# Kernel optimization log

Hardware: AMD Instinct MI355X
Metric: run time of the kernel (lower is better)

## Reference

```python
import jax, jax.numpy as jnp
import numpy as np

D_MODEL = 1024
NUM_HEADS = 16
DEPTH = D_MODEL // NUM_HEADS
B, S = 2, 2048


def setup_inputs() -> dict:
    key = jax.random.key(0)
    ks = jax.random.split(key, 12)
    std = 1.0 / np.sqrt(D_MODEL)
    inp = {
        "q": jax.random.normal(ks[0], (B, S, D_MODEL), dtype=jnp.float32),
        "k": jax.random.normal(ks[1], (B, S, D_MODEL), dtype=jnp.float32),
        "v": jax.random.normal(ks[2], (B, S, D_MODEL), dtype=jnp.float32),
        "mask": jax.random.randint(ks[3], (B, 1, 1, S), 0, 2, dtype=jnp.int32),
        "wq": jax.random.normal(ks[4], (D_MODEL, D_MODEL), dtype=jnp.float32) * std,
        "bq": jnp.zeros((D_MODEL,), dtype=jnp.float32),
        "wk": jax.random.normal(ks[5], (D_MODEL, D_MODEL), dtype=jnp.float32) * std,
        "bk": jnp.zeros((D_MODEL,), dtype=jnp.float32),
        "wv": jax.random.normal(ks[6], (D_MODEL, D_MODEL), dtype=jnp.float32) * std,
        "bv": jnp.zeros((D_MODEL,), dtype=jnp.float32),
        "wo": jax.random.normal(ks[7], (D_MODEL, D_MODEL), dtype=jnp.float32) * std,
        "bo": jnp.zeros((D_MODEL,), dtype=jnp.float32),
    }
    return inp


def _split_heads(x):
    # (B, S, D) -> (B, H, S, depth)
    b, s, _ = x.shape
    return x.reshape(b, s, NUM_HEADS, DEPTH).transpose(0, 2, 1, 3)


def reference(q, k, v, mask, wq, bq, wk, bk, wv, bv, wo, bo):
    qh = _split_heads(q @ wq + bq)   # (B,H,S,depth)
    kh = _split_heads(k @ wk + bk)
    vh = _split_heads(v @ wv + bv)
    scale = 1.0 / jnp.sqrt(jnp.float32(DEPTH))
    logits = jnp.einsum("bhqd,bhkd->bhqk", qh, kh) * scale  # (B,H,Sq,Sk)
    logits = logits + mask.astype(logits.dtype) * -1e9
    attn = jax.nn.softmax(logits, axis=-1)
    out = jnp.einsum("bhqk,bhkd->bhqd", attn, vh)  # (B,H,Sq,depth)
    out = out.transpose(0, 2, 1, 3).reshape(q.shape[0], -1, D_MODEL)
    return out @ wo + bo
```

## Files before the change

kernel.cpp:

```cpp
#include <hip/hip_runtime.h>
#include <hip/hip_bf16.h>
#include <stdint.h>


typedef __bf16 bf16;
typedef __bf16 bf16x8 __attribute__((ext_vector_type(8)));
typedef __bf16 bf16x4 __attribute__((ext_vector_type(4)));
typedef float  f32x4  __attribute__((ext_vector_type(4)));

#define D_MODEL 1024
#define S_LEN   2048
#define NH      16
#define DEPTH   64

#define LOG2E   1.4426950408889634f
#define QSCALE  (0.125f * LOG2E)
#define SMAX    20.0f
#define MPEN    (-30000.0f)

__device__ __forceinline__ void gload_lds16(const void* g, void* l) {
  __builtin_amdgcn_global_load_lds(
      (__attribute__((address_space(1))) void*)g,
      (__attribute__((address_space(3))) void*)l,
      16, 0, 0);
}

__global__ void probe_dtype(const uint32_t* __restrict__ qw, int* __restrict__ flag)
{
  const int t = threadIdx.x;
  int c = 0;
  for (int i = 0; i < 4; ++i) {
    uint32_t w = qw[t * 4 + i];
    uint32_t e = (w >> 7) & 0xFF;
    c += (e >= 90 && e <= 150) ? 1 : 0;
  }
  for (int s = 1; s < 64; s <<= 1) c += __shfl_xor(c, s);
  if (t == 0) *flag = (c > 160) ? 1 : 0;
}

__global__ __launch_bounds__(256) void prep_qkv(
    const void* __restrict__ q, const void* __restrict__ k,
    const void* __restrict__ v,
    bf16* __restrict__ qb, bf16* __restrict__ kb, bf16* __restrict__ vb,
    const int* __restrict__ flagp)
{
  if (*flagp) return;
  const void* src; bf16* dst;
  switch (blockIdx.z) {
    case 0:  src = q; dst = qb; break;
    case 1:  src = k; dst = kb; break;
    default: src = v; dst = vb; break;
  }
  const size_t idx = ((size_t)blockIdx.x * 256 + threadIdx.x) * 8;
  const float* s = (const float*)src + idx;
  f32x4 a = *(const f32x4*)(s);
  f32x4 b = *(const f32x4*)(s + 4);
  bf16x8 o;
  for (int i = 0; i < 4; ++i) { o[i] = (bf16)a[i]; o[4 + i] = (bf16)b[i]; }
  *(bf16x8*)(dst + idx) = o;
}

__global__ __launch_bounds__(256) void prep_w(
    const void* __restrict__ w0, const void* __restrict__ w1,
    const void* __restrict__ w2, const void* __restrict__ w3,
    bf16* __restrict__ t0, bf16* __restrict__ t1,
    bf16* __restrict__ t2, bf16* __restrict__ t3,
    const int* __restrict__ flagp)
{
  const int flag = *flagp;
  const void* W; bf16* T;
  switch (blockIdx.z) {
    case 0:  W = w0; T = t0; break;
    case 1:  W = w1; T = t1; break;
    case 2:  W = w2; T = t2; break;
    default: W = w3; T = t3; break;
  }
  const float sc = (blockIdx.z == 0) ? QSCALE : 1.0f;
  __shared__ float tile[32][33];
  const int tx = threadIdx.x;
  const int x0 = blockIdx.x * 32;
  const int y0 = blockIdx.y * 32;
  for (int i = threadIdx.y; i < 32; i += 8) {
    const size_t gi = (size_t)(y0 + i) * D_MODEL + x0 + tx;
    tile[i][tx] = flag ? (float)((const bf16*)W)[gi] : ((const float*)W)[gi];
  }
  __syncthreads();
  for (int i = threadIdx.y; i < 32; i += 8)
    T[(size_t)(x0 + i) * D_MODEL + y0 + tx] = (bf16)(tile[tx][i] * sc);
}

__global__ __launch_bounds__(256) void prep_bias(
    const void* __restrict__ b0, const void* __restrict__ b1,
    const void* __restrict__ b2, const void* __restrict__ b3,
    bf16* __restrict__ o0, bf16* __restrict__ o1,
    bf16* __restrict__ o2, bf16* __restrict__ o3,
    const int* __restrict__ flagp)
{
  const int flag = *flagp;
  const void* B; bf16* O;
  switch (blockIdx.x) {
    case 0:  B = b0; O = o0; break;
    case 1:  B = b1; O = o1; break;
    case 2:  B = b2; O = o2; break;
    default: B = b3; O = o3; break;
  }
  const float sc = (blockIdx.x == 0) ? QSCALE : 1.0f;
  for (int j = 0; j < 4; ++j) {
    const int i = threadIdx.x + j * 256;
    const float v = flag ? (float)((const bf16*)B)[i] : ((const float*)B)[i];
    O[i] = (bf16)(v * sc);
  }
}

struct GArgs {
  const bf16* A;
  const void* Araw;
  const bf16* BT;
  const bf16* bias;
  void* out;
  int mode;
};

__global__ __launch_bounds__(256) void gemm_bt(GArgs g0, GArgs g1, GArgs g2,
                                               const int* __restrict__ flagp)
{
  GArgs g = (blockIdx.z == 0) ? g0 : ((blockIdx.z == 1) ? g1 : g2);
  const int flag = *flagp;
  const bf16* A = flag ? (const bf16*)g.Araw : g.A;

  __shared__ __align__(16) bf16 As[128 * 32];
  __shared__ __align__(16) bf16 Bs[128 * 32];
  const int tid  = threadIdx.x;
  const int wave = tid >> 6, lane = tid & 63;
  const int quad = lane >> 4, l16 = lane & 15;
  const int m0 = blockIdx.y * 128, n0 = blockIdx.x * 128;
  const int wm = (wave >> 1) * 64, wn = (wave & 1) * 64;
  const int srow = lane >> 2;
  const int scol = (lane & 3) * 8;

  f32x4 acc[4][4] = {};

  const bf16* Ag = A    + (size_t)(m0 + wave * 32 + srow) * D_MODEL + scol;
  const bf16* Bg = g.BT + (size_t)(n0 + wave * 32 + srow) * D_MODEL + scol;
  bf16* Asw = As + (wave * 32) * 32;
  bf16* Bsw = Bs + (wave * 32) * 32;

  for (int kt = 0; kt < D_MODEL; kt += 32) {
    __syncthreads();
    gload_lds16(Ag + kt,                Asw);
    gload_lds16(Ag + kt + 16 * D_MODEL, Asw + 16 * 32);
    gload_lds16(Bg + kt,                Bsw);
    gload_lds16(Bg + kt + 16 * D_MODEL, Bsw + 16 * 32);
    __syncthreads();

    bf16x8 af[4], bfv[4];
#pragma unroll
    for (int mi = 0; mi < 4; ++mi)
      af[mi] = *(const bf16x8*)(As + (wm + mi * 16 + l16) * 32 + quad * 8);
#pragma unroll
    for (int ni = 0; ni < 4; ++ni)
      bfv[ni] = *(const bf16x8*)(Bs + (wn + ni * 16 + l16) * 32 + quad * 8);
#pragma unroll
    for (int mi = 0; mi < 4; ++mi)
#pragma unroll
      for (int ni = 0; ni < 4; ++ni)
        acc[mi][ni] = __builtin_amdgcn_mfma_f32_16x16x32_bf16(
            af[mi], bfv[ni], acc[mi][ni], 0, 0, 0);
  }

#pragma unroll
  for (int mi = 0; mi < 4; ++mi) {
#pragma unroll
    for (int ni = 0; ni < 4; ++ni) {
      const int col  = n0 + wn + ni * 16 + l16;
      const float bv = (float)g.bias[col];
      const int row0 = m0 + wm + mi * 16 + quad * 4;
      const int b = row0 >> 11, s = row0 & 2047, hh = col >> 6, d = col & 63;
      if (g.mode == 2) {
        bf16x4 pk;
#pragma unroll
        for (int r = 0; r < 4; ++r)
          pk[r] = (bf16)(acc[mi][ni][r] + bv);
        *(bf16x4*)((bf16*)g.out + ((size_t)((b * NH + hh) * DEPTH + d)) * S_LEN + s) = pk;
      } else if (g.mode == 1) {
        bf16* op = (bf16*)g.out + ((size_t)(b * NH + hh) * S_LEN + s) * DEPTH + d;
#pragma unroll
        for (int r = 0; r < 4; ++r)
          op[(size_t)r * DEPTH] = (bf16)(acc[mi][ni][r] + bv);
      } else {
        if (flag) {
          bf16* op = (bf16*)g.out + (size_t)row0 * D_MODEL + col;
#pragma unroll
          for (int r = 0; r < 4; ++r)
            op[(size_t)r * D_MODEL] = (bf16)(acc[mi][ni][r] + bv);
        } else {
          float* op = (float*)g.out + (size_t)row0 * D_MODEL + col;
#pragma unroll
          for (int r = 0; r < 4; ++r)
            op[(size_t)r * D_MODEL] = acc[mi][ni][r] + bv;
        }
      }
    }
  }
}

__global__ __launch_bounds__(256) void attn(
    const bf16* __restrict__ Qh, const bf16* __restrict__ Kh,
    const bf16* __restrict__ Vt, const int* __restrict__ mask,
    bf16* __restrict__ Oh)
{
  const int bh = blockIdx.y;
  const int b  = bh >> 4;
  const int h  = bh & 15;
  const int q0 = blockIdx.x * 64;
  const int tid = threadIdx.x, wave = tid >> 6, lane = tid & 63;
  const int quad = lane >> 4, l16 = lane & 15;

  __shared__ __align__(16) bf16 Ks[64][72];
  __shared__ __align__(16) bf16 Vts[64][72];
  __shared__ __align__(16) bf16 Ps[4][16][72];
  __shared__ float mf2[S_LEN];

  const int* mg = mask + b * S_LEN;
  for (int i = tid; i < S_LEN; i += 256)
    mf2[i] = mg[i] ? (MPEN - SMAX) : (-SMAX);

  const bf16* Qg = Qh + ((size_t)bh * S_LEN + q0 + wave * 16 + l16) * DEPTH;
  bf16x8 aq0 = *(const bf16x8*)(Qg + quad * 8);
  bf16x8 aq1 = *(const bf16x8*)(Qg + 32 + quad * 8);

  bf16x8 ones;
#pragma unroll
  for (int j = 0; j < 8; ++j) ones[j] = (bf16)1.0f;

  f32x4 o_acc[4] = {};
  f32x4 l_acc = {};

  const bf16* Kg = Kh + (size_t)bh * S_LEN * DEPTH;
  const bf16* Vg = Vt + (size_t)bh * DEPTH * S_LEN;

  for (int kb = 0; kb < S_LEN; kb += 64) {
    __syncthreads();
    for (int i = tid; i < 512; i += 256) {
      int r = i >> 3, c = (i & 7) * 8;
      *(bf16x8*)(&Ks[r][c])  = *(const bf16x8*)(Kg + (size_t)(kb + r) * DEPTH + c);
      *(bf16x8*)(&Vts[r][c]) = *(const bf16x8*)(Vg + (size_t)r * S_LEN + kb + c);
    }
    __syncthreads();

    f32x4 sacc[4] = {};
#pragma unroll
    for (int jn = 0; jn < 4; ++jn) {
      bf16x8 bk0 = *(const bf16x8*)(&Ks[jn * 16 + l16][quad * 8]);
      bf16x8 bk1 = *(const bf16x8*)(&Ks[jn * 16 + l16][32 + quad * 8]);
      sacc[jn] = __builtin_amdgcn_mfma_f32_16x16x32_bf16(aq0, bk0, sacc[jn], 0, 0, 0);
      sacc[jn] = __builtin_amdgcn_mfma_f32_16x16x32_bf16(aq1, bk1, sacc[jn], 0, 0, 0);
    }

#pragma unroll
    for (int jn = 0; jn < 4; ++jn) {
      const float mc = mf2[kb + jn * 16 + l16];
#pragma unroll
      for (int r = 0; r < 4; ++r)
        Ps[wave][quad * 4 + r][jn * 16 + l16] =
            (bf16)__builtin_amdgcn_exp2f(sacc[jn][r] + mc);
    }

    bf16x8 ap0 = *(const bf16x8*)(&Ps[wave][l16][quad * 8]);
    bf16x8 ap1 = *(const bf16x8*)(&Ps[wave][l16][32 + quad * 8]);
#pragma unroll
    for (int jd = 0; jd < 4; ++jd) {
      bf16x8 bv0 = *(const bf16x8*)(&Vts[jd * 16 + l16][quad * 8]);
      bf16x8 bv1 = *(const bf16x8*)(&Vts[jd * 16 + l16][32 + quad * 8]);
      o_acc[jd] = __builtin_amdgcn_mfma_f32_16x16x32_bf16(ap0, bv0, o_acc[jd], 0, 0, 0);
      o_acc[jd] = __builtin_amdgcn_mfma_f32_16x16x32_bf16(ap1, bv1, o_acc[jd], 0, 0, 0);
    }
    l_acc = __builtin_amdgcn_mfma_f32_16x16x32_bf16(ap0, ones, l_acc, 0, 0, 0);
    l_acc = __builtin_amdgcn_mfma_f32_16x16x32_bf16(ap1, ones, l_acc, 0, 0, 0);
  }

#pragma unroll
  for (int r = 0; r < 4; ++r) {
    const int s = q0 + wave * 16 + quad * 4 + r;
    const float inv = 1.f / l_acc[r];
#pragma unroll
    for (int jd = 0; jd < 4; ++jd) {
      const int d = jd * 16 + l16;
      Oh[(size_t)(b * S_LEN + s) * D_MODEL + h * DEPTH + d] =
          (bf16)(o_acc[jd][r] * inv);
    }
  }
}

extern "C" void kernel_launch(void* const* d_in, const int* in_sizes, int n_in,
                              void* d_out, int out_size, void* d_ws, size_t ws_size,
                              hipStream_t stream)
{
  const void* q    = d_in[0];
  const void* k    = d_in[1];
  const void* v    = d_in[2];
  const int*  mask = (const int*)d_in[3];
  const void* wq   = d_in[4];
  const void* bq   = d_in[5];
  const void* wk   = d_in[6];
  const void* bk   = d_in[7];
  const void* wv   = d_in[8];
  const void* bv   = d_in[9];
  const void* wo   = d_in[10];
  const void* bo   = d_in[11];

  char* ws = (char*)d_ws;
  const size_t MB = 1u << 20;
  bf16* Qh  = (bf16*)(ws + 0 * MB);
  bf16* Kh  = (bf16*)(ws + 8 * MB);
  bf16* Vt  = (bf16*)(ws + 16 * MB);
  bf16* Oh  = (bf16*)(ws + 24 * MB);
  bf16* wqT = (bf16*)(ws + 32 * MB);
  bf16* wkT = (bf16*)(ws + 34 * MB);
  bf16* wvT = (bf16*)(ws + 36 * MB);
  bf16* woT = (bf16*)(ws + 38 * MB);
  bf16* bqb = (bf16*)(ws + 40 * MB);
  bf16* bkb = (bf16*)(ws + 40 * MB + 4096);
  bf16* bvb = (bf16*)(ws + 40 * MB + 8192);
  bf16* bob = (bf16*)(ws + 40 * MB + 12288);
  int*  flag = (int*)(ws + 40 * MB + 32768);
  bf16* qb  = (bf16*)(ws + 41 * MB);
  bf16* kb_ = (bf16*)(ws + 49 * MB);
  bf16* vb_ = (bf16*)(ws + 57 * MB);

  probe_dtype<<<1, 64, 0, stream>>>((const uint32_t*)q, flag);

  prep_qkv<<<dim3(2048, 1, 3), 256, 0, stream>>>(q, k, v, qb, kb_, vb_, flag);
  prep_w<<<dim3(32, 32, 4), dim3(32, 8), 0, stream>>>(
      wq, wk, wv, wo, wqT, wkT, wvT, woT, flag);
  prep_bias<<<4, 256, 0, stream>>>(bq, bk, bv, bo, bqb, bkb, bvb, bob, flag);

  GArgs gq{qb,  q,  wqT, bqb, Qh, 1};
  GArgs gk{kb_, k,  wkT, bkb, Kh, 1};
  GArgs gv{vb_, v,  wvT, bvb, Vt, 2};
  gemm_bt<<<dim3(8, 32, 3), 256, 0, stream>>>(gq, gk, gv, flag);

  attn<<<dim3(32, 32), 256, 0, stream>>>(Qh, Kh, Vt, mask, Oh);

  GArgs go{Oh, Oh, woT, bob, d_out, 0};
  gemm_bt<<<dim3(8, 32, 1), 256, 0, stream>>>(go, go, go, flag);
}
```

Measured before the change: 273.9 us.

## Compact unmasked keys/values and skip masked key blocks in attention

Adds a prefix-scan kernel over the mask that assigns each unmasked key a compacted position and counts them per batch. The K/V projection epilogues scatter only unmasked rows into compacted buffers, so attention loops only over the padded count of valid keys and no longer reads the mask. Attention also processes 128 queries per block (32 per wave) so each K/V tile is reused across twice as many queries. Masked keys contribute about exp(-1e9)=0 in the reference, so skipping them is exact for any mask; the cost is an extra launch and scattered stores in the GEMM epilogue.

```diff
diff --git a/kernel.cpp b/kernel.cpp
--- a/kernel.cpp
+++ b/kernel.cpp
@@ -16,7 +16,7 @@
 #define LOG2E   1.4426950408889634f
 #define QSCALE  (0.125f * LOG2E)
 #define SMAX    20.0f
-#define MPEN    (-30000.0f)
+#define PADPEN  (-30000.0f)
 
 __device__ __forceinline__ void gload_lds16(const void* g, void* l) {
   __builtin_amdgcn_global_load_lds(
@@ -36,6 +36,38 @@
   }
   for (int s = 1; s < 64; s <<= 1) c += __shfl_xor(c, s);
   if (t == 0) *flag = (c > 160) ? 1 : 0;
+}
+
+__global__ __launch_bounds__(256) void scan_mask(
+    const int* __restrict__ mask, int* __restrict__ cpos, int* __restrict__ nb)
+{
+  const int b = blockIdx.x;
+  const int t = threadIdx.x;
+  const int lane = t & 63, wv = t >> 6;
+  __shared__ int wsum[4];
+
+  int vals[8], s = 0;
+#pragma unroll
+  for (int j = 0; j < 8; ++j) {
+    vals[j] = (mask[b * S_LEN + t * 8 + j] == 0) ? 1 : 0;
+    s += vals[j];
+  }
+  int acc = s;
+  for (int off = 1; off < 64; off <<= 1) {
+    int u = __shfl_up(acc, off);
+    if (lane >= off) acc += u;
+  }
+  if (lane == 63) wsum[wv] = acc;
+  __syncthreads();
+  int base = 0;
+  for (int w = 0; w < 4; ++w) base += (w < wv) ? wsum[w] : 0;
+  int ex = base + acc - s;
+#pragma unroll
+  for (int j = 0; j < 8; ++j) {
+    cpos[b * S_LEN + t * 8 + j] = vals[j] ? ex : -1;
+    ex += vals[j];
+  }
+  if (t == 255) nb[b] = base + acc;
 }
 
 __global__ __launch_bounds__(256) void prep_qkv(
@@ -118,6 +150,7 @@
   const bf16* BT;
   const bf16* bias;
   void* out;
+  const int* cpos;
   int mode;
 };
 
@@ -170,18 +203,28 @@
 
 #pragma unroll
   for (int mi = 0; mi < 4; ++mi) {
+    const int row0 = m0 + wm + mi * 16 + quad * 4;
+    const int b = row0 >> 11, s = row0 & 2047;
+    int cp[4];
+    if (g.mode >= 2) {
+#pragma unroll
+      for (int r = 0; r < 4; ++r) cp[r] = g.cpos[b * S_LEN + s + r];
+    }
 #pragma unroll
     for (int ni = 0; ni < 4; ++ni) {
       const int col  = n0 + wn + ni * 16 + l16;
       const float bv = (float)g.bias[col];
-      const int row0 = m0 + wm + mi * 16 + quad * 4;
-      const int b = row0 >> 11, s = row0 & 2047, hh = col >> 6, d = col & 63;
-      if (g.mode == 2) {
-        bf16x4 pk;
+      const int hh = col >> 6, d = col & 63;
+      if (g.mode == 3) {
+        bf16* base = (bf16*)g.out + (size_t)(b * NH + hh) * S_LEN * DEPTH + d;
 #pragma unroll
         for (int r = 0; r < 4; ++r)
-          pk[r] = (bf16)(acc[mi][ni][r] + bv);
-        *(bf16x4*)((bf16*)g.out + ((size_t)((b * NH + hh) * DEPTH + d)) * S_LEN + s) = pk;
+          if (cp[r] >= 0) base[(size_t)cp[r] * DEPTH] = (bf16)(acc[mi][ni][r] + bv);
+      } else if (g.mode == 2) {
+        bf16* base = (bf16*)g.out + ((size_t)(b * NH + hh) * DEPTH + d) * S_LEN;
+#pragma unroll
+        for (int r = 0; r < 4; ++r)
+          if (cp[r] >= 0) base[cp[r]] = (bf16)(acc[mi][ni][r] + bv);
       } else if (g.mode == 1) {
         bf16* op = (bf16*)g.out + ((size_t)(b * NH + hh) * S_LEN + s) * DEPTH + d;
 #pragma unroll
@@ -205,41 +248,41 @@
 }
 
 __global__ __launch_bounds__(256) void attn(
-    const bf16* __restrict__ Qh, const bf16* __restrict__ Kh,
-    const bf16* __restrict__ Vt, const int* __restrict__ mask,
+    const bf16* __restrict__ Qh, const bf16* __restrict__ Kc,
+    const bf16* __restrict__ Vc, const int* __restrict__ nbp,
     bf16* __restrict__ Oh)
 {
   const int bh = blockIdx.y;
   const int b  = bh >> 4;
   const int h  = bh & 15;
-  const int q0 = blockIdx.x * 64;
+  const int q0 = blockIdx.x * 128;
   const int tid = threadIdx.x, wave = tid >> 6, lane = tid & 63;
   const int quad = lane >> 4, l16 = lane & 15;
 
   __shared__ __align__(16) bf16 Ks[64][72];
   __shared__ __align__(16) bf16 Vts[64][72];
-  __shared__ __align__(16) bf16 Ps[4][16][72];
-  __shared__ float mf2[S_LEN];
-
-  const int* mg = mask + b * S_LEN;
-  for (int i = tid; i < S_LEN; i += 256)
-    mf2[i] = mg[i] ? (MPEN - SMAX) : (-SMAX);
-
-  const bf16* Qg = Qh + ((size_t)bh * S_LEN + q0 + wave * 16 + l16) * DEPTH;
-  bf16x8 aq0 = *(const bf16x8*)(Qg + quad * 8);
-  bf16x8 aq1 = *(const bf16x8*)(Qg + 32 + quad * 8);
+  __shared__ __align__(16) bf16 Ps[4][32][72];
+
+  const int nbv = nbp[b];
+  const int nb_pad = (nbv + 63) & ~63;
+
+  const bf16* Qg = Qh + ((size_t)bh * S_LEN + q0 + wave * 32) * DEPTH;
+  bf16x8 aq00 = *(const bf16x8*)(Qg + (size_t)l16 * DEPTH + quad * 8);
+  bf16x8 aq01 = *(const bf16x8*)(Qg + (size_t)l16 * DEPTH + 32 + quad * 8);
+  bf16x8 aq10 = *(const bf16x8*)(Qg + (size_t)(16 + l16) * DEPTH + quad * 8);
+  bf16x8 aq11 = *(const bf16x8*)(Qg + (size_t)(16 + l16) * DEPTH + 32 + quad * 8);
 
   bf16x8 ones;
 #pragma unroll
   for (int j = 0; j < 8; ++j) ones[j] = (bf16)1.0f;
 
-  f32x4 o_acc[4] = {};
-  f32x4 l_acc = {};
-
-  const bf16* Kg = Kh + (size_t)bh * S_LEN * DEPTH;
-  const bf16* Vg = Vt + (size_t)bh * DEPTH * S_LEN;
-
-  for (int kb = 0; kb < S_LEN; kb += 64) {
+  f32x4 o_acc[2][4] = {};
+  f32x4 l_acc[2] = {};
+
+  const bf16* Kg = Kc + (size_t)bh * S_LEN * DEPTH;
+  const bf16* Vg = Vc + (size_t)bh * DEPTH * S_LEN;
+
+  for (int kb = 0; kb < nb_pad; kb += 64) {
     __syncthreads();
     for (int i = tid; i < 512; i += 256) {
       int r = i >> 3, c = (i & 7) * 8;
@@ -248,46 +291,60 @@
     }
     __syncthreads();
 
-    f32x4 sacc[4] = {};
+    f32x4 sacc[2][4] = {};
 #pragma unroll
     for (int jn = 0; jn < 4; ++jn) {
       bf16x8 bk0 = *(const bf16x8*)(&Ks[jn * 16 + l16][quad * 8]);
       bf16x8 bk1 = *(const bf16x8*)(&Ks[jn * 16 + l16][32 + quad * 8]);
-      sacc[jn] = __builtin_amdgcn_mfma_f32_16x16x32_bf16(aq0, bk0, sacc[jn], 0, 0, 0);
-      sacc[jn] = __builtin_amdgcn_mfma_f32_16x16x32_bf16(aq1, bk1, sacc[jn], 0, 0, 0);
+      sacc[0][jn] = __builtin_amdgcn_mfma_f32_16x16x32_bf16(aq00, bk0, sacc[0][jn], 0, 0, 0);
+      sacc[0][jn] = __builtin_amdgcn_mfma_f32_16x16x32_bf16(aq01, bk1, sacc[0][jn], 0, 0, 0);
+      sacc[1][jn] = __builtin_amdgcn_mfma_f32_16x16x32_bf16(aq10, bk0, sacc[1][jn], 0, 0, 0);
+      sacc[1][jn] = __builtin_amdgcn_mfma_f32_16x16x32_bf16(aq11, bk1, sacc[1][jn], 0, 0, 0);
     }
 
 #pragma unroll
     for (int jn = 0; jn < 4; ++jn) {
-      const float mc = mf2[kb + jn * 16 + l16];
-#pragma unroll
-      for (int r = 0; r < 4; ++r)
-        Ps[wave][quad * 4 + r][jn * 16 + l16] =
-            (bf16)__builtin_amdgcn_exp2f(sacc[jn][r] + mc);
-    }
-
-    bf16x8 ap0 = *(const bf16x8*)(&Ps[wave][l16][quad * 8]);
-    bf16x8 ap1 = *(const bf16x8*)(&Ps[wave][l16][32 + quad * 8]);
+      const int key = kb + jn * 16 + l16;
+      const float pen = (key < nbv) ? (-SMAX) : PADPEN;
+#pragma unroll
+      for (int qs = 0; qs < 2; ++qs)
+#pragma unroll
+        for (int r = 0; r < 4; ++r)
+          Ps[wave][qs * 16 + quad * 4 + r][jn * 16 + l16] =
+              (bf16)__builtin_amdgcn_exp2f(sacc[qs][jn][r] + pen);
+    }
+
+    bf16x8 ap00 = *(const bf16x8*)(&Ps[wave][l16][quad * 8]);
+    bf16x8 ap01 = *(const bf16x8*)(&Ps[wave][l16][32 + quad * 8]);
+    bf16x8 ap10 = *(const bf16x8*)(&Ps[wave][16 + l16][quad * 8]);
+    bf16x8 ap11 = *(const bf16x8*)(&Ps[wave][16 + l16][32 + quad * 8]);
 #pragma unroll
     for (int jd = 0; jd < 4; ++jd) {
       bf16x8 bv0 = *(const bf16x8*)(&Vts[jd * 16 + l16][quad * 8]);
       bf16x8 bv1 = *(const bf16x8*)(&Vts[jd * 16 + l16][32 + quad * 8]);
-      o_acc[jd] = __builtin_amdgcn_mfma_f32_16x16x32_bf16(ap0, bv0, o_acc[jd], 0, 0, 0);
-      o_acc[jd] = __builtin_amdgcn_mfma_f32_16x16x32_bf16(ap1, bv1, o_acc[jd], 0, 0, 0);
-    }
-    l_acc = __builtin_amdgcn_mfma_f32_16x16x32_bf16(ap0, ones, l_acc, 0, 0, 0);
-    l_acc = __builtin_amdgcn_mfma_f32_16x16x32_bf16(ap1, ones, l_acc, 0, 0, 0);
-  }
-
-#pragma unroll
-  for (int r = 0; r < 4; ++r) {
-    const int s = q0 + wave * 16 + quad * 4 + r;
-    const float inv = 1.f / l_acc[r];
-#pragma unroll
-    for (int jd = 0; jd < 4; ++jd) {
-      const int d = jd * 16 + l16;
-      Oh[(size_t)(b * S_LEN + s) * D_MODEL + h * DEPTH + d] =
-          (bf16)(o_acc[jd][r] * inv);
+      o_acc[0][jd] = __builtin_amdgcn_mfma_f32_16x16x32_bf16(ap00, bv0, o_acc[0][jd], 0, 0, 0);
+      o_acc[0][jd] = __builtin_amdgcn_mfma_f32_16x16x32_bf16(ap01, bv1, o_acc[0][jd], 0, 0, 0);
+      o_acc[1][jd] = __builtin_amdgcn_mfma_f32_16x16x32_bf16(ap10, bv0, o_acc[1][jd], 0, 0, 0);
+      o_acc[1][jd] = __builtin_amdgcn_mfma_f32_16x16x32_bf16(ap11, bv1, o_acc[1][jd], 0, 0, 0);
+    }
+    l_acc[0] = __builtin_amdgcn_mfma_f32_16x16x32_bf16(ap00, ones, l_acc[0], 0, 0, 0);
+    l_acc[0] = __builtin_amdgcn_mfma_f32_16x16x32_bf16(ap01, ones, l_acc[0], 0, 0, 0);
+    l_acc[1] = __builtin_amdgcn_mfma_f32_16x16x32_bf16(ap10, ones, l_acc[1], 0, 0, 0);
+    l_acc[1] = __builtin_amdgcn_mfma_f32_16x16x32_bf16(ap11, ones, l_acc[1], 0, 0, 0);
+  }
+
+#pragma unroll
+  for (int qs = 0; qs < 2; ++qs) {
+#pragma unroll
+    for (int r = 0; r < 4; ++r) {
+      const int s = q0 + wave * 32 + qs * 16 + quad * 4 + r;
+      const float inv = 1.f / l_acc[qs][r];
+#pragma unroll
+      for (int jd = 0; jd < 4; ++jd) {
+        const int d = jd * 16 + l16;
+        Oh[(size_t)(b * S_LEN + s) * D_MODEL + h * DEPTH + d] =
+            (bf16)(o_acc[qs][jd][r] * inv);
+      }
     }
   }
 }
@@ -312,8 +369,8 @@
   char* ws = (char*)d_ws;
   const size_t MB = 1u << 20;
   bf16* Qh  = (bf16*)(ws + 0 * MB);
-  bf16* Kh  = (bf16*)(ws + 8 * MB);
-  bf16* Vt  = (bf16*)(ws + 16 * MB);
+  bf16* Kc  = (bf16*)(ws + 8 * MB);
+  bf16* Vc  = (bf16*)(ws + 16 * MB);
   bf16* Oh  = (bf16*)(ws + 24 * MB);
   bf16* wqT = (bf16*)(ws + 32 * MB);
   bf16* wkT = (bf16*)(ws + 34 * MB);
@@ -324,24 +381,27 @@
   bf16* bvb = (bf16*)(ws + 40 * MB + 8192);
   bf16* bob = (bf16*)(ws + 40 * MB + 12288);
   int*  flag = (int*)(ws + 40 * MB + 32768);
+  int*  cpos = (int*)(ws + 40 * MB + 65536);
+  int*  nb   = (int*)(ws + 40 * MB + 65536 + 16384);
   bf16* qb  = (bf16*)(ws + 41 * MB);
   bf16* kb_ = (bf16*)(ws + 49 * MB);
   bf16* vb_ = (bf16*)(ws + 57 * MB);
 
   probe_dtype<<<1, 64, 0, stream>>>((const uint32_t*)q, flag);
+  scan_mask<<<2, 256, 0, stream>>>(mask, cpos, nb);
 
   prep_qkv<<<dim3(2048, 1, 3), 256, 0, stream>>>(q, k, v, qb, kb_, vb_, flag);
   prep_w<<<dim3(32, 32, 4), dim3(32, 8), 0, stream>>>(
       wq, wk, wv, wo, wqT, wkT, wvT, woT, flag);
   prep_bias<<<4, 256, 0, stream>>>(bq, bk, bv, bo, bqb, bkb, bvb, bob, flag);
 
-  GArgs gq{qb,  q,  wqT, bqb, Qh, 1};
-  GArgs gk{kb_, k,  wkT, bkb, Kh, 1};
-  GArgs gv{vb_, v,  wvT, bvb, Vt, 2};
+  GArgs gq{qb,  q,  wqT, bqb, Qh, nullptr, 1};
+  GArgs gk{kb_, k,  wkT, bkb, Kc, cpos,    3};
+  GArgs gv{vb_, v,  wvT, bvb, Vc, cpos,    2};
   gemm_bt<<<dim3(8, 32, 3), 256, 0, stream>>>(gq, gk, gv, flag);
 
-  attn<<<dim3(32, 32), 256, 0, stream>>>(Qh, Kh, Vt, mask, Oh);
-
-  GArgs go{Oh, Oh, woT, bob, d_out, 0};
+  attn<<<dim3(16, 32), 256, 0, stream>>>(Qh, Kc, Vc, nb, Oh);
+
+  GArgs go{Oh, Oh, woT, bob, d_out, nullptr, 0};
   gemm_bt<<<dim3(8, 32, 1), 256, 0, stream>>>(go, go, go, flag);
 }
```

Result: faster. 240.9 us (-12.1%).
